# Performance work log

Hardware: AMD Instinct MI355X
Metric: run time of the kernel (lower is better)

Reference implementation:

```python
import jax, jax.numpy as jnp
import numpy as np

N_HEAD = 16
HEAD_SIZE = 64  # n_embd // n_head = 1024 // 16


def setup_inputs() -> dict:
    key = jax.random.key(0)
    k1, k2 = jax.random.split(key)
    B, T, C = 2, 2048, 1024
    x = jax.random.normal(k1, (B, T, C), dtype=jnp.float32)
    w_attn = jax.random.normal(k2, (C, 3 * C), dtype=jnp.float32) * (C ** -0.5)
    b_attn = jnp.zeros((3 * C,), dtype=jnp.float32)
    return {"x": x, "w_attn": w_attn, "b_attn": b_attn}


def reference(x, w_attn, b_attn):
    B, T, C = x.shape
    qkv = x @ w_attn + b_attn  # [B, T, 3C]
    q, k, v = jnp.split(qkv, 3, axis=-1)
    # [B, T, H, D] -> [B, H, T, D]
    def heads(t):
        return t.reshape(B, T, N_HEAD, HEAD_SIZE).transpose(0, 2, 1, 3)
    q, k, v = heads(q), heads(k), heads(v)
    scale = HEAD_SIZE ** -0.5
    wei = jnp.einsum('bhqd,bhkd->bhqk', q, k) * scale  # [B, H, T, T]
    causal = jnp.tril(jnp.ones((T, T), dtype=bool))
    wei = jnp.where(causal, wei, -jnp.inf)
    wei = jax.nn.softmax(wei, axis=-1)
    out = jnp.einsum('bhqk,bhkd->bhqd', wei, v)  # [B, H, T, D]
    out = out.transpose(0, 2, 1, 3).reshape(B, T, C)
    return out
```

## Files before the change

### kernel.cpp

```cpp
#include <hip/hip_runtime.h>
#include <hip/hip_bf16.h>

#define BSZ 2
#define SEQ 2048
#define CDIM 1024
#define NHEAD 16
#define HDIM 64
#define M_GEMM (BSZ * SEQ)
#define N_GEMM (3 * CDIM)
#define K_GEMM CDIM
#define QK_PITCH (2 * CDIM)

typedef __attribute__((ext_vector_type(8))) short short8;
typedef __attribute__((ext_vector_type(4))) short short4v;
typedef __attribute__((ext_vector_type(4))) float f32x4;

__device__ __forceinline__ short bf16_rn(float f) {
    unsigned u = __builtin_bit_cast(unsigned, f);
    u += 0x7FFF + ((u >> 16) & 1);
    return (short)(u >> 16);
}

__device__ __forceinline__ void gl2lds16(const short* g, short* l) {
    __builtin_amdgcn_global_load_lds(
        (const __attribute__((address_space(1))) unsigned int*)g,
        (__attribute__((address_space(3))) unsigned int*)l, 16, 0, 0);
}

__global__ __launch_bounds__(256) void cvt_x(const float* __restrict__ X,
                                             short* __restrict__ Xb) {
    size_t idx = ((size_t)blockIdx.x * 256 + threadIdx.x) * 8;
    float4 a = *(const float4*)&X[idx];
    float4 b = *(const float4*)&X[idx + 4];
    short8 o;
    o[0] = bf16_rn(a.x); o[1] = bf16_rn(a.y); o[2] = bf16_rn(a.z); o[3] = bf16_rn(a.w);
    o[4] = bf16_rn(b.x); o[5] = bf16_rn(b.y); o[6] = bf16_rn(b.z); o[7] = bf16_rn(b.w);
    *(short8*)&Xb[idx] = o;
}

__global__ __launch_bounds__(256) void cvt_wT(const float* __restrict__ W,
                                              short* __restrict__ WT) {
    __shared__ short T[64][72];
    const int n0 = blockIdx.x * 64;
    const int k0 = blockIdx.y * 64;
    const int tid = threadIdx.x;
#pragma unroll
    for (int pass = 0; pass < 4; ++pass) {
        int i = pass * 256 + tid;
        int kr = i >> 4;
        int n4 = i & 15;
        float4 v = *(const float4*)&W[(size_t)(k0 + kr) * N_GEMM + n0 + n4 * 4];
        T[n4 * 4 + 0][kr] = bf16_rn(v.x);
        T[n4 * 4 + 1][kr] = bf16_rn(v.y);
        T[n4 * 4 + 2][kr] = bf16_rn(v.z);
        T[n4 * 4 + 3][kr] = bf16_rn(v.w);
    }
    __syncthreads();
#pragma unroll
    for (int pass = 0; pass < 2; ++pass) {
        int o = pass * 256 + tid;
        int nr = o >> 3;
        int c8 = o & 7;
        *(short8*)&WT[(size_t)(n0 + nr) * K_GEMM + k0 + c8 * 8] =
            *(const short8*)&T[nr][c8 * 8];
    }
}

#define GBK 32

__global__ __launch_bounds__(256) void qkv_gemm_mfma(const short* __restrict__ A,
                                                     const short* __restrict__ Bt,
                                                     const float* __restrict__ bias,
                                                     short* __restrict__ Yqk,
                                                     short* __restrict__ Yv) {
    __shared__ short Asl[128 * GBK];
    __shared__ short Bsl[128 * GBK];

    const int tid = threadIdx.x;
    const int w = tid >> 6;
    const int l16 = tid & 15;
    const int quad = (tid & 63) >> 4;
    const int wm = w >> 1, wn = w & 1;
    const int m0 = blockIdx.y * 128;
    const int n0 = blockIdx.x * 128;

    f32x4 acc[4][4];
#pragma unroll
    for (int i = 0; i < 4; ++i)
#pragma unroll
        for (int j = 0; j < 4; ++j) acc[i][j] = (f32x4){0.f, 0.f, 0.f, 0.f};

    const int cid0 = tid, cid1 = 256 + tid;
    const int ar0 = cid0 >> 2, as0 = (cid0 & 3) ^ (ar0 & 3);
    const int ar1 = cid1 >> 2, as1 = (cid1 & 3) ^ (ar1 & 3);
    const short* Ap0 = A + (size_t)(m0 + ar0) * K_GEMM + as0 * 8;
    const short* Ap1 = A + (size_t)(m0 + ar1) * K_GEMM + as1 * 8;
    const short* Bp0 = Bt + (size_t)(n0 + ar0) * K_GEMM + as0 * 8;
    const short* Bp1 = Bt + (size_t)(n0 + ar1) * K_GEMM + as1 * 8;
    short* Al0 = &Asl[(w * 64) * 8];
    short* Al1 = &Asl[(256 + w * 64) * 8];
    short* Bl0 = &Bsl[(w * 64) * 8];
    short* Bl1 = &Bsl[(256 + w * 64) * 8];

    const int fsw = quad ^ (l16 & 3);

    for (int kt = 0; kt < K_GEMM; kt += GBK) {
        __syncthreads();
        gl2lds16(Ap0 + kt, Al0);
        gl2lds16(Ap1 + kt, Al1);
        gl2lds16(Bp0 + kt, Bl0);
        gl2lds16(Bp1 + kt, Bl1);
        __syncthreads();

        short8 af[4], bfr[4];
#pragma unroll
        for (int i = 0; i < 4; ++i) {
            int r = wm * 64 + i * 16 + l16;
            af[i] = *(const short8*)&Asl[(r * 4 + fsw) * 8];
        }
#pragma unroll
        for (int j = 0; j < 4; ++j) {
            int r = wn * 64 + j * 16 + l16;
            bfr[j] = *(const short8*)&Bsl[(r * 4 + fsw) * 8];
        }
#pragma unroll
        for (int i = 0; i < 4; ++i)
#pragma unroll
            for (int j = 0; j < 4; ++j)
                acc[i][j] = __builtin_amdgcn_mfma_f32_16x16x32_bf16(
                    af[i], bfr[j], acc[i][j], 0, 0, 0);
    }

    if (n0 >= 2 * CDIM) {
#pragma unroll
        for (int i = 0; i < 4; ++i) {
            int row0 = m0 + wm * 64 + i * 16 + quad * 4;
#pragma unroll
            for (int j = 0; j < 4; ++j) {
                int colg = n0 + wn * 64 + j * 16 + l16;
                float bb = bias[colg];
                short4v pk;
#pragma unroll
                for (int r = 0; r < 4; ++r) pk[r] = bf16_rn(acc[i][j][r] + bb);
                *(short4v*)&Yv[(size_t)(colg - 2 * CDIM) * M_GEMM + row0] = pk;
            }
        }
    } else {
        const float qs = (n0 < CDIM) ? 0.125f : 1.0f;
#pragma unroll
        for (int i = 0; i < 4; ++i)
#pragma unroll
            for (int r = 0; r < 4; ++r) {
                int row = m0 + wm * 64 + i * 16 + quad * 4 + r;
#pragma unroll
                for (int j = 0; j < 4; ++j) {
                    int colg = n0 + wn * 64 + j * 16 + l16;
                    Yqk[(size_t)row * QK_PITCH + colg] =
                        bf16_rn((acc[i][j][r] + bias[colg]) * qs);
                }
            }
    }
}

__global__ __launch_bounds__(256) void attn_mfma(const short* __restrict__ qk,
                                                 const short* __restrict__ vT,
                                                 float* __restrict__ out) {
    const int b = blockIdx.z;
    const int h = blockIdx.y;
    const int qt = gridDim.x - 1 - blockIdx.x;
    const int tid = threadIdx.x;
    const int w = tid >> 6;
    const int lane = tid & 63;
    const int quad = lane >> 4;
    const int l16 = lane & 15;
    const int q0 = qt * 64;

    __shared__ short Ks[64 * 64];
    __shared__ short Vt[64 * 64];
    __shared__ short Ps[4 * 16 * 64];

    int koff[2], voff[2];
    short *ksb[2], *vtb[2];
#pragma unroll
    for (int p = 0; p < 2; ++p) {
        int cid = p * 256 + w * 64 + lane;
        int row = cid >> 3;
        int c = (cid & 7) ^ (row & 7);
        koff[p] = row * QK_PITCH + c * 8;
        voff[p] = row * M_GEMM + c * 8;
        ksb[p] = &Ks[(p * 256 + w * 64) * 8];
        vtb[p] = &Vt[(p * 256 + w * 64) * 8];
    }

    const short* qrow = qk + (size_t)(b * SEQ + q0 + w * 16 + l16) * QK_PITCH + h * HDIM;
    short8 aq[2];
    aq[0] = *(const short8*)(qrow + quad * 8);
    aq[1] = *(const short8*)(qrow + 32 + quad * 8);

    float l_run[4] = {0.f, 0.f, 0.f, 0.f};
    f32x4 o_acc[4];
#pragma unroll
    for (int dt = 0; dt < 4; ++dt) o_acc[dt] = (f32x4){0.f, 0.f, 0.f, 0.f};

    const int rowg0 = q0 + w * 16 + quad * 4;
    const short* kb0 = qk + (size_t)(b * SEQ) * QK_PITCH + CDIM + h * HDIM;
    const short* vb0 = vT + (size_t)(h * HDIM) * M_GEMM + b * SEQ;

    const int ksl = l16 & 7;
    short* PsW = &Ps[w * 1024];

    for (int kt = 0; kt <= qt; ++kt) {
        const short* kbase = kb0 + (size_t)kt * 64 * QK_PITCH;
        const short* vbase = vb0 + kt * 64;

        __syncthreads();
        gl2lds16(kbase + koff[0], ksb[0]);
        gl2lds16(kbase + koff[1], ksb[1]);
        gl2lds16(vbase + voff[0], vtb[0]);
        gl2lds16(vbase + voff[1], vtb[1]);
        __syncthreads();

        f32x4 s[4];
#pragma unroll
        for (int nt = 0; nt < 4; ++nt) s[nt] = (f32x4){0.f, 0.f, 0.f, 0.f};
#pragma unroll
        for (int nt = 0; nt < 4; ++nt)
#pragma unroll
            for (int ks = 0; ks < 2; ++ks) {
                short8 bk = *(const short8*)&Ks[(nt * 16 + l16) * 64 +
                                                ((ks * 4 + quad) ^ ksl) * 8];
                s[nt] = __builtin_amdgcn_mfma_f32_16x16x32_bf16(aq[ks], bk, s[nt], 0, 0, 0);
            }

        if (kt < qt) {
#pragma unroll
            for (int r = 0; r < 4; ++r) {
                const int qr = quad * 4 + r;
                float lsum = 0.f;
#pragma unroll
                for (int nt = 0; nt < 4; ++nt) {
                    float pp = __expf(s[nt][r]);
                    lsum += pp;
                    int slot = (nt * 2 + (l16 >> 3)) ^ (qr & 7);
                    PsW[qr * 64 + slot * 8 + (l16 & 7)] = bf16_rn(pp);
                }
                l_run[r] += lsum;
            }
        } else {
            const int keyb = kt * 64 + l16;
#pragma unroll
            for (int r = 0; r < 4; ++r) {
                const int qr = quad * 4 + r;
                const int rowg = rowg0 + r;
                float lsum = 0.f;
#pragma unroll
                for (int nt = 0; nt < 4; ++nt) {
                    float pp = __expf(s[nt][r]);
                    pp = ((keyb + nt * 16) > rowg) ? 0.f : pp;
                    lsum += pp;
                    int slot = (nt * 2 + (l16 >> 3)) ^ (qr & 7);
                    PsW[qr * 64 + slot * 8 + (l16 & 7)] = bf16_rn(pp);
                }
                l_run[r] += lsum;
            }
        }

#pragma unroll
        for (int dt = 0; dt < 4; ++dt)
#pragma unroll
            for (int ks = 0; ks < 2; ++ks) {
                short8 ap = *(const short8*)&PsW[l16 * 64 + ((ks * 4 + quad) ^ ksl) * 8];
                short8 bv = *(const short8*)&Vt[(dt * 16 + l16) * 64 +
                                                ((ks * 4 + quad) ^ ksl) * 8];
                o_acc[dt] = __builtin_amdgcn_mfma_f32_16x16x32_bf16(ap, bv, o_acc[dt], 0, 0, 0);
            }
    }

#pragma unroll
    for (int r = 0; r < 4; ++r) {
        float l = l_run[r];
#pragma unroll
        for (int off = 1; off < 16; off <<= 1)
            l += __shfl_xor(l, off);
        float inv = 1.f / l;
        int row = q0 + w * 16 + quad * 4 + r;
        float* optr = out + (size_t)(b * SEQ + row) * CDIM + h * HDIM;
#pragma unroll
        for (int dt = 0; dt < 4; ++dt)
            optr[dt * 16 + l16] = o_acc[dt][r] * inv;
    }
}

extern "C" void kernel_launch(void* const* d_in, const int* in_sizes, int n_in,
                              void* d_out, int out_size, void* d_ws, size_t ws_size,
                              hipStream_t stream) {
    const float* x      = (const float*)d_in[0];
    const float* w_attn = (const float*)d_in[1];
    const float* b_attn = (const float*)d_in[2];
    float* out = (float*)d_out;

    short* qk  = (short*)d_ws;
    short* vT  = (short*)((char*)d_ws + 16777216);
    short* xb  = (short*)((char*)d_ws + 25165824);
    short* wT  = (short*)((char*)d_ws + 33554432);

    cvt_x<<<M_GEMM * K_GEMM / 2048, 256, 0, stream>>>(x, xb);
    dim3 gt(N_GEMM / 64, K_GEMM / 64);
    cvt_wT<<<gt, 256, 0, stream>>>(w_attn, wT);

    dim3 g1(N_GEMM / 128, M_GEMM / 128);
    qkv_gemm_mfma<<<g1, 256, 0, stream>>>(xb, wT, b_attn, qk, vT);

    dim3 g2(SEQ / 64, NHEAD, BSZ);
    attn_mfma<<<g2, 256, 0, stream>>>(qk, vT, out);
}
```

Before: 187.9 us.

## Compute transposed S so P stays in registers via lane shuffles instead of LDS

The attention kernel now computes S^T (keys as MFMA rows, queries as columns), so each lane holds four consecutive keys for one query. The P tile is packed to bf16 pairs and redistributed with cross-lane shuffles into the MFMA B-operand layout, which removes the per-wave LDS staging buffer and its write/read round trip. It also makes the row-sum reduction cheaper and lets the output be written with float4 stores. In exchange it adds shuffle instructions and selects per tile, and relies on the shuffle mapping being correct.

```diff
diff --git a/kernel.cpp b/kernel.cpp
--- a/kernel.cpp
+++ b/kernel.cpp
@@ -14,11 +14,20 @@
 typedef __attribute__((ext_vector_type(8))) short short8;
 typedef __attribute__((ext_vector_type(4))) short short4v;
 typedef __attribute__((ext_vector_type(4))) float f32x4;
+typedef __attribute__((ext_vector_type(4))) unsigned int u32x4;
 
 __device__ __forceinline__ short bf16_rn(float f) {
     unsigned u = __builtin_bit_cast(unsigned, f);
     u += 0x7FFF + ((u >> 16) & 1);
     return (short)(u >> 16);
+}
+
+__device__ __forceinline__ unsigned pack_bf16x2(float lo, float hi) {
+    unsigned a = __builtin_bit_cast(unsigned, lo);
+    a += 0x7FFF + ((a >> 16) & 1);
+    unsigned b = __builtin_bit_cast(unsigned, hi);
+    b += 0x7FFF + ((b >> 16) & 1);
+    return (a >> 16) | (b & 0xFFFF0000u);
 }
 
 __device__ __forceinline__ void gl2lds16(const short* g, short* l) {
@@ -177,7 +186,6 @@
 
     __shared__ short Ks[64 * 64];
     __shared__ short Vt[64 * 64];
-    __shared__ short Ps[4 * 16 * 64];
 
     int koff[2], voff[2];
     short *ksb[2], *vtb[2];
@@ -197,17 +205,19 @@
     aq[0] = *(const short8*)(qrow + quad * 8);
     aq[1] = *(const short8*)(qrow + 32 + quad * 8);
 
-    float l_run[4] = {0.f, 0.f, 0.f, 0.f};
+    float l_run = 0.f;
     f32x4 o_acc[4];
 #pragma unroll
     for (int dt = 0; dt < 4; ++dt) o_acc[dt] = (f32x4){0.f, 0.f, 0.f, 0.f};
 
-    const int rowg0 = q0 + w * 16 + quad * 4;
+    const int rowq = q0 + w * 16 + l16;
     const short* kb0 = qk + (size_t)(b * SEQ) * QK_PITCH + CDIM + h * HDIM;
     const short* vb0 = vT + (size_t)(h * HDIM) * M_GEMM + b * SEQ;
 
     const int ksl = l16 & 7;
-    short* PsW = &Ps[w * 1024];
+    const int src0 = ((2 * quad + 0) & 3) * 16 + l16;
+    const int src1 = ((2 * quad + 1) & 3) * 16 + l16;
+    const bool hi = (quad >> 1) != 0;
 
     for (int kt = 0; kt <= qt; ++kt) {
         const short* kbase = kb0 + (size_t)kt * 64 * QK_PITCH;
@@ -222,72 +232,74 @@
 
         f32x4 s[4];
 #pragma unroll
-        for (int nt = 0; nt < 4; ++nt) s[nt] = (f32x4){0.f, 0.f, 0.f, 0.f};
-#pragma unroll
-        for (int nt = 0; nt < 4; ++nt)
+        for (int mt = 0; mt < 4; ++mt) s[mt] = (f32x4){0.f, 0.f, 0.f, 0.f};
+#pragma unroll
+        for (int mt = 0; mt < 4; ++mt)
 #pragma unroll
             for (int ks = 0; ks < 2; ++ks) {
-                short8 bk = *(const short8*)&Ks[(nt * 16 + l16) * 64 +
+                short8 ak = *(const short8*)&Ks[(mt * 16 + l16) * 64 +
                                                 ((ks * 4 + quad) ^ ksl) * 8];
-                s[nt] = __builtin_amdgcn_mfma_f32_16x16x32_bf16(aq[ks], bk, s[nt], 0, 0, 0);
-            }
-
+                s[mt] = __builtin_amdgcn_mfma_f32_16x16x32_bf16(ak, aq[ks], s[mt], 0, 0, 0);
+            }
+
+        unsigned pk[4][2];
         if (kt < qt) {
 #pragma unroll
-            for (int r = 0; r < 4; ++r) {
-                const int qr = quad * 4 + r;
-                float lsum = 0.f;
-#pragma unroll
-                for (int nt = 0; nt < 4; ++nt) {
-                    float pp = __expf(s[nt][r]);
-                    lsum += pp;
-                    int slot = (nt * 2 + (l16 >> 3)) ^ (qr & 7);
-                    PsW[qr * 64 + slot * 8 + (l16 & 7)] = bf16_rn(pp);
-                }
-                l_run[r] += lsum;
+            for (int mt = 0; mt < 4; ++mt) {
+                float p0 = __expf(s[mt][0]);
+                float p1 = __expf(s[mt][1]);
+                float p2 = __expf(s[mt][2]);
+                float p3 = __expf(s[mt][3]);
+                l_run += (p0 + p1) + (p2 + p3);
+                pk[mt][0] = pack_bf16x2(p0, p1);
+                pk[mt][1] = pack_bf16x2(p2, p3);
             }
         } else {
-            const int keyb = kt * 64 + l16;
-#pragma unroll
-            for (int r = 0; r < 4; ++r) {
-                const int qr = quad * 4 + r;
-                const int rowg = rowg0 + r;
-                float lsum = 0.f;
-#pragma unroll
-                for (int nt = 0; nt < 4; ++nt) {
-                    float pp = __expf(s[nt][r]);
-                    pp = ((keyb + nt * 16) > rowg) ? 0.f : pp;
-                    lsum += pp;
-                    int slot = (nt * 2 + (l16 >> 3)) ^ (qr & 7);
-                    PsW[qr * 64 + slot * 8 + (l16 & 7)] = bf16_rn(pp);
-                }
-                l_run[r] += lsum;
-            }
-        }
-
-#pragma unroll
-        for (int dt = 0; dt < 4; ++dt)
-#pragma unroll
-            for (int ks = 0; ks < 2; ++ks) {
-                short8 ap = *(const short8*)&PsW[l16 * 64 + ((ks * 4 + quad) ^ ksl) * 8];
-                short8 bv = *(const short8*)&Vt[(dt * 16 + l16) * 64 +
+            const int keyb = kt * 64 + quad * 4;
+#pragma unroll
+            for (int mt = 0; mt < 4; ++mt) {
+                float p0 = (keyb + mt * 16 + 0 > rowq) ? 0.f : __expf(s[mt][0]);
+                float p1 = (keyb + mt * 16 + 1 > rowq) ? 0.f : __expf(s[mt][1]);
+                float p2 = (keyb + mt * 16 + 2 > rowq) ? 0.f : __expf(s[mt][2]);
+                float p3 = (keyb + mt * 16 + 3 > rowq) ? 0.f : __expf(s[mt][3]);
+                l_run += (p0 + p1) + (p2 + p3);
+                pk[mt][0] = pack_bf16x2(p0, p1);
+                pk[mt][1] = pack_bf16x2(p2, p3);
+            }
+        }
+
+#pragma unroll
+        for (int ks = 0; ks < 2; ++ks) {
+            u32x4 bf;
+#pragma unroll
+            for (int pj = 0; pj < 4; ++pj) {
+                const int g = pj >> 1, rp = pj & 1;
+                const int src = g ? src1 : src0;
+                unsigned va = (unsigned)__shfl((int)pk[2 * ks + 0][rp], src);
+                unsigned vb = (unsigned)__shfl((int)pk[2 * ks + 1][rp], src);
+                bf[pj] = hi ? vb : va;
+            }
+            short8 bp = __builtin_bit_cast(short8, bf);
+#pragma unroll
+            for (int dt = 0; dt < 4; ++dt) {
+                short8 av = *(const short8*)&Vt[(dt * 16 + l16) * 64 +
                                                 ((ks * 4 + quad) ^ ksl) * 8];
-                o_acc[dt] = __builtin_amdgcn_mfma_f32_16x16x32_bf16(ap, bv, o_acc[dt], 0, 0, 0);
-            }
-    }
-
-#pragma unroll
-    for (int r = 0; r < 4; ++r) {
-        float l = l_run[r];
-#pragma unroll
-        for (int off = 1; off < 16; off <<= 1)
-            l += __shfl_xor(l, off);
-        float inv = 1.f / l;
-        int row = q0 + w * 16 + quad * 4 + r;
-        float* optr = out + (size_t)(b * SEQ + row) * CDIM + h * HDIM;
-#pragma unroll
-        for (int dt = 0; dt < 4; ++dt)
-            optr[dt * 16 + l16] = o_acc[dt][r] * inv;
+                o_acc[dt] = __builtin_amdgcn_mfma_f32_16x16x32_bf16(av, bp, o_acc[dt], 0, 0, 0);
+            }
+        }
+    }
+
+    float l = l_run;
+    l += __shfl_xor(l, 16);
+    l += __shfl_xor(l, 32);
+    const float inv = 1.f / l;
+    float* optr = out + (size_t)(b * SEQ + rowq) * CDIM + h * HDIM;
+#pragma unroll
+    for (int dt = 0; dt < 4; ++dt) {
+        f32x4 v = o_acc[dt];
+        float4 st;
+        st.x = v[0] * inv; st.y = v[1] * inv; st.z = v[2] * inv; st.w = v[3] * inv;
+        *(float4*)&optr[dt * 16 + quad * 4] = st;
     }
 }
 
```

Measured after the change: 198.0 us. +5.3%, slower.
